# Kernel optimization log

Measured on AMD Instinct MI355X. Metric: run time of the kernel, lower is better.

## Reference

```python
import jax, jax.numpy as jnp
import numpy as np

EPS = 1e-5

def conv2d(x, w, stride=1, padding=0, bias=None):
    out = jax.lax.conv_general_dilated(
        x, w, (stride, stride), [(padding, padding), (padding, padding)],
        dimension_numbers=('NCHW', 'OIHW', 'NCHW'))
    if bias is not None:
        out = out + bias[None, :, None, None]
    return out

def bn_relu(x, gamma, beta, mean, var):
    scale = gamma / jnp.sqrt(var + EPS)
    return jax.nn.relu(x * scale[None, :, None, None]
                       + (beta - mean * scale)[None, :, None, None])

def deform_conv(x, wp, bp, wc, ks, pad, stride):
    # Canonical DeformConv2d (v1, modulation=False) from pytorch-deform-conv-v2.
    b, c, H, W = x.shape
    N = ks * ks
    offset = conv2d(x, wp, stride=stride, padding=1, bias=bp)        # (b,2N,h,w)
    h, w = offset.shape[2], offset.shape[3]
    xp = jnp.pad(x, ((0, 0), (0, 0), (pad, pad), (pad, pad)))        # zero_padding
    Hp, Wp = H + 2 * pad, W + 2 * pad
    off = offset.transpose(0, 2, 3, 1)                               # (b,h,w,2N)
    rng = jnp.arange(-(ks - 1) // 2, (ks - 1) // 2 + 1, dtype=x.dtype)
    pnx, pny = jnp.meshgrid(rng, rng, indexing='ij')
    pnx, pny = pnx.reshape(-1), pny.reshape(-1)                      # (N,)
    p0x = jnp.arange(1, h * stride + 1, stride, dtype=x.dtype)       # torch starts at 1
    p0y = jnp.arange(1, w * stride + 1, stride, dtype=x.dtype)
    px = p0x[None, :, None, None] + pnx[None, None, None, :] + off[..., :N]  # (b,h,w,N)
    py = p0y[None, None, :, None] + pny[None, None, None, :] + off[..., N:]
    qx0 = jnp.floor(jax.lax.stop_gradient(px))
    qy0 = jnp.floor(jax.lax.stop_gradient(py))
    qx0c = jnp.clip(qx0, 0, Hp - 1).astype(jnp.int32)
    qx1c = jnp.clip(qx0 + 1, 0, Hp - 1).astype(jnp.int32)
    qy0c = jnp.clip(qy0, 0, Wp - 1).astype(jnp.int32)
    qy1c = jnp.clip(qy0 + 1, 0, Wp - 1).astype(jnp.int32)
    pxc = jnp.clip(px, 0, Hp - 1)
    pyc = jnp.clip(py, 0, Wp - 1)
    fx0 = qx0c.astype(x.dtype); fx1 = qx1c.astype(x.dtype)
    fy0 = qy0c.astype(x.dtype); fy1 = qy1c.astype(x.dtype)
    g_lt = (1 + (fx0 - pxc)) * (1 + (fy0 - pyc))
    g_rb = (1 - (fx1 - pxc)) * (1 - (fy1 - pyc))
    g_lb = (1 + (fx0 - pxc)) * (1 - (fy1 - pyc))
    g_rt = (1 - (fx1 - pxc)) * (1 + (fy0 - pyc))
    xf = xp.reshape(b, c, Hp * Wp)
    def gather(qx, qy):
        idx = (qx * Wp + qy).reshape(b, 1, h * w * N)
        return jnp.take_along_axis(xf, idx, axis=2).reshape(b, c, h, w, N)
    x_off = (g_lt[:, None] * gather(qx0c, qy0c)
             + g_rb[:, None] * gather(qx1c, qy1c)
             + g_lb[:, None] * gather(qx0c, qy1c)
             + g_rt[:, None] * gather(qx1c, qy0c))                   # (b,c,h,w,N)
    # stride=ks conv over the reshaped (h*ks, w*ks) map == einsum over sample slot n
    return jnp.einsum('bchwn,ocn->bohw', x_off, wc.reshape(wc.shape[0], c, N))

def setup_inputs() -> dict:
    key = jax.random.key(0)
    ks = iter(jax.random.split(key, 40))
    def nrm(shape, scale):
        return jax.random.normal(next(ks), shape, dtype=jnp.float32) * scale
    def he(shape):  # fan_in = prod of all but first dim
        return nrm(shape, float(np.sqrt(2.0 / np.prod(shape[1:]))))
    def bn(c):
        return (jnp.ones((c,), jnp.float32) + nrm((c,), 0.05),  # gamma
                nrm((c,), 0.05),                                 # beta
                nrm((c,), 0.1),                                  # running mean
                jax.random.uniform(next(ks), (c,), jnp.float32, 0.5, 1.5))  # var
    inp = {'x': jax.random.normal(next(ks), (256, 3, 32, 32), dtype=jnp.float32)}
    inp['w1'] = he((32, 3, 3, 3)); inp['b1'] = nrm((32,), 0.01)
    inp['g1'], inp['be1'], inp['m1'], inp['v1'] = bn(32)
    inp['wp2'] = nrm((18, 32, 3, 3), 0.01); inp['bp2'] = nrm((18,), 0.001)
    inp['wc2'] = he((64, 32, 3, 3))
    inp['g2'], inp['be2'], inp['m2'], inp['v2'] = bn(64)
    inp['wp3'] = nrm((18, 64, 3, 3), 0.01); inp['bp3'] = nrm((18,), 0.001)
    inp['wc3'] = he((128, 64, 3, 3))
    inp['g3'], inp['be3'], inp['m3'], inp['v3'] = bn(128)
    inp['wp4'] = nrm((18, 128, 3, 3), 0.01); inp['bp4'] = nrm((18,), 0.001)
    inp['wc4'] = he((128, 128, 3, 3))
    inp['g4'], inp['be4'], inp['m4'], inp['v4'] = bn(128)
    inp['wcls'] = nrm((100, 128), float(1.0 / np.sqrt(128)))
    inp['bcls'] = nrm((100,), 0.01)
    return inp

def reference(x, w1, b1, g1, be1, m1, v1,
              wp2, bp2, wc2, g2, be2, m2, v2,
              wp3, bp3, wc3, g3, be3, m3, v3,
              wp4, bp4, wc4, g4, be4, m4, v4,
              wcls, bcls):
    h = bn_relu(conv2d(x, w1, stride=1, padding=1, bias=b1), g1, be1, m1, v1)   # (b,32,32,32)
    h = bn_relu(deform_conv(h, wp2, bp2, wc2, 3, 1, 2), g2, be2, m2, v2)        # (b,64,16,16)
    h = bn_relu(deform_conv(h, wp3, bp3, wc3, 3, 1, 1), g3, be3, m3, v3)        # (b,128,16,16)
    h = bn_relu(deform_conv(h, wp4, bp4, wc4, 3, 1, 2), g4, be4, m4, v4)        # (b,128,8,8)
    h = jnp.mean(h, axis=(2, 3))                                                # avg_pool2d(8) -> (b,128)
    return h @ wcls.T + bcls[None, :]
```

## Files before the change

### kernel.cpp

```cpp
#include <hip/hip_runtime.h>
#include <math.h>

#define BN_EPS 1e-5f

typedef __attribute__((ext_vector_type(4))) float f4;
typedef __attribute__((ext_vector_type(4))) int i4v;
typedef __attribute__((ext_vector_type(8))) short short8;
typedef __attribute__((ext_vector_type(4))) float f32x4;
typedef _Float16 half4v __attribute__((ext_vector_type(4)));

__device__ inline unsigned short f2bf(float f) {
    unsigned int u = __builtin_bit_cast(unsigned int, f);
    return (unsigned short)((u + 0x7FFFu + ((u >> 16) & 1u)) >> 16);
}
__device__ inline float blo(int u) { return __builtin_bit_cast(float, (int)(u << 16)); }
__device__ inline float bhi(int u) { return __builtin_bit_cast(float, (int)(u & 0xffff0000)); }
__device__ inline int pkbf_fast(float hi, float lo) {
    unsigned uh = __builtin_bit_cast(unsigned, hi) + 0x8000u;
    unsigned ul = __builtin_bit_cast(unsigned, lo) + 0x8000u;
    return (int)__builtin_amdgcn_perm(uh, ul, 0x07060302u);
}

struct CvtSeg { const float* src; unsigned short* dst; int oreal, c, kpad, end; };
struct CvtArgs { CvtSeg s[7]; };

__global__ __launch_bounds__(256)
void cvt_all(CvtArgs a)
{
    int idx = blockIdx.x * 256 + threadIdx.x;
    int base = 0;
    #pragma unroll
    for (int i = 0; i < 7; ++i) {
        if (idx < a.s[i].end) {
            int local = idx - base;
            int kpad = a.s[i].kpad, c = a.s[i].c;
            int o = local / kpad, k = local - o * kpad;
            unsigned short val = 0;
            if (o < a.s[i].oreal && k < 9 * c) {
                int n = k / c, cc = k - n * c;
                val = f2bf(a.s[i].src[(o * c + cc) * 9 + n]);
            }
            a.s[i].dst[local] = val;
            return;
        }
        base = a.s[i].end;
    }
}

__global__ __launch_bounds__(256)
void conv1_tile(const float* __restrict__ x, const unsigned short* __restrict__ wq,
                const float* __restrict__ bias, const float* __restrict__ g,
                const float* __restrict__ be, const float* __restrict__ m,
                const float* __restrict__ v, unsigned short* __restrict__ out)
{
    __shared__ __align__(16) float img[3072];
    __shared__ __align__(16) unsigned short wt[32 * 40];
    __shared__ float scb[32], shb[32];
    const int tid = threadIdx.x;
    const int b = blockIdx.x >> 2;
    const int qtr = blockIdx.x & 3;
    if (tid < 32) {
        float sc = g[tid] * rsqrtf(v[tid] + BN_EPS);
        scb[tid] = sc;
        shb[tid] = be[tid] - m[tid] * sc + bias[tid] * sc;
    }
    *(ushort4*)&wt[(tid >> 3) * 40 + (tid & 7) * 4] =
        *(const ushort4*)(wq + (tid >> 3) * 32 + (tid & 7) * 4);
    const float* xb = x + (size_t)b * 3072;
    #pragma unroll
    for (int r = 0; r < 3; ++r) {
        int idx = r * 256 + tid;
        *(f4*)&img[idx * 4] = *(const f4*)(xb + idx * 4);
    }
    __syncthreads();
    const int wid = tid >> 6, lane = tid & 63, quad = lane >> 4, m16 = lane & 15;
    short8 af0 = *(const short8*)&wt[m16 * 40 + quad * 8];
    short8 af1 = *(const short8*)&wt[(16 + m16) * 40 + quad * 8];
    #pragma unroll
    for (int it = 0; it < 4; ++it) {
        int pix = qtr * 256 + it * 64 + wid * 16 + m16;
        int i = pix >> 5, j = pix & 31;
        short8 bfrag;
        #pragma unroll
        for (int jj = 0; jj < 8; ++jj) {
            int k = quad * 8 + jj;
            float val = 0.f;
            if (k < 27) {
                int n = k / 3, c = k - n * 3;
                int u = i - 1 + n / 3, vv = j - 1 + n % 3;
                if (u >= 0 && u < 32 && vv >= 0 && vv < 32)
                    val = img[c * 1024 + u * 32 + vv];
            }
            bfrag[jj] = (short)f2bf(val);
        }
        f32x4 a0 = {0.f,0.f,0.f,0.f}, a1 = {0.f,0.f,0.f,0.f};
        a0 = __builtin_amdgcn_mfma_f32_16x16x32_bf16(af0, bfrag, a0, 0, 0, 0);
        a1 = __builtin_amdgcn_mfma_f32_16x16x32_bf16(af1, bfrag, a1, 0, 0, 0);
        unsigned short* op = out + ((size_t)b * 1024 + pix) * 32;
        ushort4 s0, s1;
        #pragma unroll
        for (int rr = 0; rr < 4; ++rr) {
            int o0 = quad * 4 + rr, o1 = 16 + quad * 4 + rr;
            ((unsigned short*)&s0)[rr] = f2bf(fmaxf(fmaf(a0[rr], scb[o0], shb[o0]), 0.f));
            ((unsigned short*)&s1)[rr] = f2bf(fmaxf(fmaf(a1[rr], scb[o1], shb[o1]), 0.f));
        }
        *(ushort4*)(op + quad * 4) = s0;
        *(ushort4*)(op + 16 + quad * 4) = s1;
    }
}

template<int C, int OREAL, int OPAD, int H, int W, int OH, int OW, int S, int MTILE>
__global__ __launch_bounds__(256, 4)
void dconv_slim(const unsigned short* __restrict__ xact,
                const unsigned short* __restrict__ wp, const float* __restrict__ bp,
                const unsigned short* __restrict__ wc,
                const float* __restrict__ g, const float* __restrict__ be,
                const float* __restrict__ m, const float* __restrict__ v,
                unsigned short* __restrict__ out)
{
    constexpr int K = C * 9;
    constexpr int KCH = C / 32;
    constexpr int OT = OPAD / 64;
    constexpr int ST = MTILE / 16;
    constexpr int PWP = MTILE / 2;
    constexpr int STP = PWP / 16;
    constexpr int CP = C + 8;
    constexpr int GL = C / 8;
    constexpr int NGRP = 256 / GL;
    constexpr int NT = MTILE / NGRP;
    constexpr int OHW = OH * OW;
    constexpr int HWC = H * W * C;
    constexpr int Hp = H + 2, Wpp = W + 2;
    static_assert(MTILE % NGRP == 0 && OPAD % 64 == 0 && STP >= 1, "tiling");

    __shared__ __align__(16) unsigned short xo[2][MTILE * CP];
    __shared__ __align__(8) ushort4   tab_p[MTILE][9];
    __shared__ __align__(8) _Float16  tab_h[MTILE][9][4];
    __shared__ _Float16 off_lds[MTILE][20];
    __shared__ int imgb[MTILE];
    __shared__ float scb[OPAD], shb[OPAD];

    const int tid = threadIdx.x;
    const int p0 = blockIdx.x * MTILE;

    if (tid < MTILE) imgb[tid] = ((p0 + tid) / OHW) * HWC;
    for (int o = tid; o < OREAL; o += 256) {
        float sc = g[o] * rsqrtf(v[o] + BN_EPS);
        scb[o] = sc;
        shb[o] = be[o] - m[o] * sc;
    }
    for (int e = tid; e < MTILE * 9; e += 256) {
        int lp = e / 9, n = e % 9;
        int p = p0 + lp;
        int rem = p % OHW;
        int i = rem / OW, j = rem % OW;
        int u = i * S - 1 + n / 3, vv = j * S - 1 + n % 3;
        bool ok = (u >= 0 && u < H && vv >= 0 && vv < W);
        ushort4 tp;
        tp.x = ok ? (unsigned short)((u * W + vv) * C) : (unsigned short)0;
        tp.y = ok ? (unsigned short)0xFFFF : (unsigned short)0;
        tp.z = 0; tp.w = 0;
        tab_p[lp][n] = tp;
    }
    __syncthreads();

    const int gl = tid % GL, grp = tid / GL;
    const int wid = tid >> 6, lane = tid & 63, quad = lane >> 4, m16 = lane & 15;

    {
        const int ogp = wid & 1;
        const int pgp = wid >> 1;
        const int obp = ogp * 16;
        const int pbp = pgp * PWP;
        i4v Tp[NT];
        auto issueA = [&](int n) {
            #pragma unroll
            for (int it = 0; it < NT; ++it) {
                const int pix = it * NGRP + grp;
                Tp[it] = *(const i4v*)(xact + imgb[pix] + gl * 8 + (int)tab_p[pix][n].x);
            }
        };
        auto commitA = [&](int n, int buf) {
            #pragma unroll
            for (int it = 0; it < NT; ++it) {
                const int pix = it * NGRP + grp;
                int mask = (int)(short)tab_p[pix][n].y;
                i4v R;
                #pragma unroll
                for (int e2 = 0; e2 < 4; ++e2) R[e2] = Tp[it][e2] & mask;
                *(i4v*)&xo[buf][pix * CP + gl * 8] = R;
            }
        };
        auto loadWp = [&](int n, short8* wf) {
            #pragma unroll
            for (int ch = 0; ch < KCH; ++ch)
                wf[ch] = *(const short8*)(wp + (size_t)(obp + m16) * K
                                          + n * C + ch * 32 + quad * 8);
        };
        f32x4 accp[STP];
        #pragma unroll
        for (int st = 0; st < STP; ++st) accp[st] = (f32x4){0.f, 0.f, 0.f, 0.f};
        short8 wfA[KCH], wfB[KCH];
        issueA(0);
        loadWp(0, wfA);
        commitA(0, 0);
        __syncthreads();
        for (int n = 0; n < 9; ++n) {
            const int cur = n & 1;
            if (n < 8) { issueA(n + 1); loadWp(n + 1, wfB); }
            #pragma unroll
            for (int ch = 0; ch < KCH; ++ch)
                #pragma unroll
                for (int st = 0; st < STP; ++st) {
                    short8 bf = *(const short8*)&xo[cur][(pbp + st * 16 + m16) * CP
                                                        + ch * 32 + quad * 8];
                    accp[st] = __builtin_amdgcn_mfma_f32_16x16x32_bf16(
                        wfA[ch], bf, accp[st], 0, 0, 0);
                }
            if (n < 8) {
                commitA(n + 1, cur ^ 1);
                #pragma unroll
                for (int ch = 0; ch < KCH; ++ch) wfA[ch] = wfB[ch];
            }
            __syncthreads();
        }
        #pragma unroll
        for (int st = 0; st < STP; ++st) {
            int pix = pbp + st * 16 + m16;
            #pragma unroll
            for (int rr = 0; rr < 4; ++rr) {
                int o = obp + quad * 4 + rr;
                if (o < 18) off_lds[pix][o] = (_Float16)(accp[st][rr] + bp[o]);
            }
        }
    }
    __syncthreads();

    for (int e = tid; e < MTILE * 9; e += 256) {
        int lp = e / 9, n = e % 9;
        int p = p0 + lp;
        int rem = p % OHW;
        int i = rem / OW, j = rem % OW;
        float ox = (float)off_lds[lp][n];
        float oy = (float)off_lds[lp][9 + n];
        float px = (float)(i * S + n / 3) + ox;
        float py = (float)(j * S + n % 3) + oy;
        int qx0 = (int)floorf(px), qy0 = (int)floorf(py);
        int x0 = min(max(qx0, 0), Hp - 1), x1 = min(max(qx0 + 1, 0), Hp - 1);
        int y0 = min(max(qy0, 0), Wpp - 1), y1 = min(max(qy0 + 1, 0), Wpp - 1);
        float pxc = fminf(fmaxf(px, 0.f), (float)(Hp - 1));
        float pyc = fminf(fmaxf(py, 0.f), (float)(Wpp - 1));
        float gx0 = 1.f + ((float)x0 - pxc), gx1 = 1.f - ((float)x1 - pxc);
        float gy0 = 1.f + ((float)y0 - pyc), gy1 = 1.f - ((float)y1 - pyc);
        int u0 = x0 - 1, u1 = x1 - 1, v0 = y0 - 1, v1 = y1 - 1;
        bool k0 = (u0 >= 0 && u0 < H && v0 >= 0 && v0 < W);
        bool k1 = (u1 >= 0 && u1 < H && v1 >= 0 && v1 < W);
        bool k2 = (u0 >= 0 && u0 < H && v1 >= 0 && v1 < W);
        bool k3 = (u1 >= 0 && u1 < H && v0 >= 0 && v0 < W);
        ushort4 tp;
        tp.x = k0 ? (unsigned short)((u0 * W + v0) * C) : (unsigned short)0;
        tp.y = k1 ? (unsigned short)((u1 * W + v1) * C) : (unsigned short)0;
        tp.z = k2 ? (unsigned short)((u0 * W + v1) * C) : (unsigned short)0;
        tp.w = k3 ? (unsigned short)((u1 * W + v0) * C) : (unsigned short)0;
        tab_p[lp][n] = tp;
        half4v hw;
        hw[0] = (_Float16)(k0 ? gx0 * gy0 : 0.f);
        hw[1] = (_Float16)(k1 ? gx1 * gy1 : 0.f);
        hw[2] = (_Float16)(k2 ? gx0 * gy1 : 0.f);
        hw[3] = (_Float16)(k3 ? gx1 * gy0 : 0.f);
        *(half4v*)&tab_h[lp][n][0] = hw;
    }
    __syncthreads();

    {
        const int obase = wid * OT * 16;
        i4v T[NT][4];
        auto issueC = [&](int n) {
            #pragma unroll
            for (int it = 0; it < NT; ++it) {
                const int pix = it * NGRP + grp;
                const unsigned short* xb = xact + imgb[pix] + gl * 8;
                ushort4 tp = tab_p[pix][n];
                T[it][0] = *(const i4v*)(xb + tp.x);
                T[it][1] = *(const i4v*)(xb + tp.y);
                T[it][2] = *(const i4v*)(xb + tp.z);
                T[it][3] = *(const i4v*)(xb + tp.w);
            }
        };
        auto commitC = [&](int n, int buf) {
            #pragma unroll
            for (int it = 0; it < NT; ++it) {
                const int pix = it * NGRP + grp;
                half4v hw = *(const half4v*)&tab_h[pix][n][0];
                float w0 = (float)hw[0], w1 = (float)hw[1];
                float w2 = (float)hw[2], w3 = (float)hw[3];
                i4v R;
                #pragma unroll
                for (int e2 = 0; e2 < 4; ++e2) {
                    float lo = w0 * blo(T[it][0][e2]);
                    lo = fmaf(w1, blo(T[it][1][e2]), lo);
                    lo = fmaf(w2, blo(T[it][2][e2]), lo);
                    lo = fmaf(w3, blo(T[it][3][e2]), lo);
                    float hi = w0 * bhi(T[it][0][e2]);
                    hi = fmaf(w1, bhi(T[it][1][e2]), hi);
                    hi = fmaf(w2, bhi(T[it][2][e2]), hi);
                    hi = fmaf(w3, bhi(T[it][3][e2]), hi);
                    R[e2] = pkbf_fast(hi, lo);
                }
                *(i4v*)&xo[buf][pix * CP + gl * 8] = R;
            }
        };
        auto loadWc = [&](int n, short8 (*wf)[OT]) {
            #pragma unroll
            for (int ch = 0; ch < KCH; ++ch)
                #pragma unroll
                for (int t = 0; t < OT; ++t)
                    wf[ch][t] = *(const short8*)(wc + (size_t)(obase + t * 16 + m16) * K
                                                 + n * C + ch * 32 + quad * 8);
        };

        f32x4 acc[ST][OT];
        #pragma unroll
        for (int st = 0; st < ST; ++st)
            #pragma unroll
            for (int t = 0; t < OT; ++t) acc[st][t] = (f32x4){0.f, 0.f, 0.f, 0.f};

        short8 wfA[KCH][OT], wfB[KCH][OT];
        issueC(0);
        loadWc(0, wfA);
        commitC(0, 0);
        __syncthreads();

        for (int n = 0; n < 9; ++n) {
            const int cur = n & 1;
            if (n < 8) {
                issueC(n + 1);
                loadWc(n + 1, wfB);
            }
            #pragma unroll
            for (int ch = 0; ch < KCH; ++ch)
                #pragma unroll
                for (int st = 0; st < ST; ++st) {
                    short8 bf = *(const short8*)&xo[cur][(st * 16 + m16) * CP
                                                        + ch * 32 + quad * 8];
                    #pragma unroll
                    for (int t = 0; t < OT; ++t)
                        acc[st][t] = __builtin_amdgcn_mfma_f32_16x16x32_bf16(
                            wfA[ch][t], bf, acc[st][t], 0, 0, 0);
                }
            if (n < 8) {
                commitC(n + 1, cur ^ 1);
                #pragma unroll
                for (int ch = 0; ch < KCH; ++ch)
                    #pragma unroll
                    for (int t = 0; t < OT; ++t) wfA[ch][t] = wfB[ch][t];
            }
            __syncthreads();
        }

        #pragma unroll
        for (int st = 0; st < ST; ++st) {
            const int p = p0 + st * 16 + m16;
            #pragma unroll
            for (int t = 0; t < OT; ++t) {
                int o = obase + t * 16 + quad * 4;
                ushort4 s;
                #pragma unroll
                for (int rr = 0; rr < 4; ++rr)
                    ((unsigned short*)&s)[rr] =
                        f2bf(fmaxf(fmaf(acc[st][t][rr], scb[o + rr], shb[o + rr]), 0.f));
                *(ushort4*)(out + (size_t)p * OPAD + o) = s;
            }
        }
    }
}

template<int C, int OREAL, int OPAD, int H, int W, int OH, int OW, int S, int MTILE>
__global__ __launch_bounds__(256, 3)
void dconv_fat(const unsigned short* __restrict__ xact,
               const unsigned short* __restrict__ wp, const float* __restrict__ bp,
               const unsigned short* __restrict__ wc,
               const float* __restrict__ g, const float* __restrict__ be,
               const float* __restrict__ m, const float* __restrict__ v,
               unsigned short* __restrict__ out)
{
    constexpr int K = C * 9;
    constexpr int KCH = C / 32;
    constexpr int OT = OPAD / 64;
    constexpr int ST = MTILE / 16;
    constexpr int PWP = MTILE / 2;
    constexpr int STP = PWP / 16;
    constexpr int CP = C + 8;
    constexpr int GL = C / 8;
    constexpr int NGRP = 256 / GL;
    constexpr int NT = MTILE / NGRP;
    constexpr int OHW = OH * OW;
    constexpr int HWC = H * W * C;
    constexpr int Hp = H + 2, Wpp = W + 2;
    static_assert(MTILE % NGRP == 0 && OPAD % 64 == 0, "tiling");

    __shared__ __align__(16) unsigned short xo[2][MTILE * CP];
    __shared__ __align__(16) i4v tab_i[MTILE][9];
    __shared__ __align__(16) f4  tab_w[MTILE][9];
    __shared__ int tab_o[MTILE][9];
    __shared__ int tab_m[MTILE][9];
    __shared__ float off_lds[MTILE][20];
    __shared__ int imgb[MTILE];
    __shared__ float scb[OPAD], shb[OPAD];

    const int tid = threadIdx.x;
    const int p0 = blockIdx.x * MTILE;

    if (tid < MTILE) imgb[tid] = ((p0 + tid) / OHW) * HWC;
    for (int o = tid; o < OREAL; o += 256) {
        float sc = g[o] * rsqrtf(v[o] + BN_EPS);
        scb[o] = sc;
        shb[o] = be[o] - m[o] * sc;
    }
    for (int e = tid; e < MTILE * 9; e += 256) {
        int lp = e / 9, n = e % 9;
        int p = p0 + lp;
        int rem = p % OHW;
        int i = rem / OW, j = rem % OW;
        int u = i * S - 1 + n / 3, vv = j * S - 1 + n % 3;
        bool ok = (u >= 0 && u < H && vv >= 0 && vv < W);
        tab_o[lp][n] = ok ? (u * W + vv) * C : 0;
        tab_m[lp][n] = ok ? -1 : 0;
    }
    __syncthreads();

    const int gl = tid % GL, grp = tid / GL;
    const int wid = tid >> 6, lane = tid & 63, quad = lane >> 4, m16 = lane & 15;

    {
        const int ogp = wid & 1, pgp = wid >> 1;
        const int obp = ogp * 16;
        const int pbp = pgp * PWP;
        i4v Tp[NT];
        auto issueA = [&](int n) {
            #pragma unroll
            for (int it = 0; it < NT; ++it) {
                const int pix = it * NGRP + grp;
                Tp[it] = *(const i4v*)(xact + imgb[pix] + gl * 8 + tab_o[pix][n]);
            }
        };
        auto commitA = [&](int n, int buf) {
            #pragma unroll
            for (int it = 0; it < NT; ++it) {
                const int pix = it * NGRP + grp;
                int mask = tab_m[pix][n];
                i4v R;
                #pragma unroll
                for (int e2 = 0; e2 < 4; ++e2) R[e2] = Tp[it][e2] & mask;
                *(i4v*)&xo[buf][pix * CP + gl * 8] = R;
            }
        };
        auto loadWp = [&](int n, short8* wf) {
            #pragma unroll
            for (int ch = 0; ch < KCH; ++ch)
                wf[ch] = *(const short8*)(wp + (size_t)(obp + m16) * K
                                          + n * C + ch * 32 + quad * 8);
        };
        f32x4 accp[STP];
        #pragma unroll
        for (int st = 0; st < STP; ++st) accp[st] = (f32x4){0.f, 0.f, 0.f, 0.f};
        short8 wfA[KCH], wfB[KCH];
        issueA(0);
        loadWp(0, wfA);
        commitA(0, 0);
        __syncthreads();
        for (int n = 0; n < 9; ++n) {
            const int cur = n & 1;
            if (n < 8) { issueA(n + 1); loadWp(n + 1, wfB); }
            #pragma unroll
            for (int ch = 0; ch < KCH; ++ch)
                #pragma unroll
                for (int st = 0; st < STP; ++st) {
                    short8 bf = *(const short8*)&xo[cur][(pbp + st * 16 + m16) * CP
                                                        + ch * 32 + quad * 8];
                    accp[st] = __builtin_amdgcn_mfma_f32_16x16x32_bf16(
                        wfA[ch], bf, accp[st], 0, 0, 0);
                }
            if (n < 8) {
                commitA(n + 1, cur ^ 1);
                #pragma unroll
                for (int ch = 0; ch < KCH; ++ch) wfA[ch] = wfB[ch];
            }
            __syncthreads();
        }
        #pragma unroll
        for (int st = 0; st < STP; ++st) {
            int pix = pbp + st * 16 + m16;
            #pragma unroll
            for (int rr = 0; rr < 4; ++rr) {
                int o = obp + quad * 4 + rr;
                if (o < 18) off_lds[pix][o] = accp[st][rr] + bp[o];
            }
        }
    }
    __syncthreads();

    for (int e = tid; e < MTILE * 9; e += 256) {
        int lp = e / 9, n = e % 9;
        int p = p0 + lp;
        int rem = p % OHW;
        int i = rem / OW, j = rem % OW;
        float ox = off_lds[lp][n];
        float oy = off_lds[lp][9 + n];
        float px = (float)(i * S + n / 3) + ox;
        float py = (float)(j * S + n % 3) + oy;
        int qx0 = (int)floorf(px), qy0 = (int)floorf(py);
        int x0 = min(max(qx0, 0), Hp - 1), x1 = min(max(qx0 + 1, 0), Hp - 1);
        int y0 = min(max(qy0, 0), Wpp - 1), y1 = min(max(qy0 + 1, 0), Wpp - 1);
        float pxc = fminf(fmaxf(px, 0.f), (float)(Hp - 1));
        float pyc = fminf(fmaxf(py, 0.f), (float)(Wpp - 1));
        float gx0 = 1.f + ((float)x0 - pxc), gx1 = 1.f - ((float)x1 - pxc);
        float gy0 = 1.f + ((float)y0 - pyc), gy1 = 1.f - ((float)y1 - pyc);
        int u0 = x0 - 1, u1 = x1 - 1, v0 = y0 - 1, v1 = y1 - 1;
        bool k0 = (u0 >= 0 && u0 < H && v0 >= 0 && v0 < W);
        bool k1 = (u1 >= 0 && u1 < H && v1 >= 0 && v1 < W);
        bool k2 = (u0 >= 0 && u0 < H && v1 >= 0 && v1 < W);
        bool k3 = (u1 >= 0 && u1 < H && v0 >= 0 && v0 < W);
        i4v ti; f4 tw;
        ti[0] = k0 ? (u0 * W + v0) * C : 0;  tw[0] = k0 ? gx0 * gy0 : 0.f;
        ti[1] = k1 ? (u1 * W + v1) * C : 0;  tw[1] = k1 ? gx1 * gy1 : 0.f;
        ti[2] = k2 ? (u0 * W + v1) * C : 0;  tw[2] = k2 ? gx0 * gy1 : 0.f;
        ti[3] = k3 ? (u1 * W + v0) * C : 0;  tw[3] = k3 ? gx1 * gy0 : 0.f;
        tab_i[lp][n] = ti;
        tab_w[lp][n] = tw;
    }
    __syncthreads();

    {
        const int obase = wid * OT * 16;
        i4v T[NT][4];
        auto issueC = [&](int n) {
            #pragma unroll
            for (int it = 0; it < NT; ++it) {
                const int pix = it * NGRP + grp;
                const unsigned short* xb = xact + imgb[pix] + gl * 8;
                i4v ti = tab_i[pix][n];
                T[it][0] = *(const i4v*)(xb + ti[0]);
                T[it][1] = *(const i4v*)(xb + ti[1]);
                T[it][2] = *(const i4v*)(xb + ti[2]);
                T[it][3] = *(const i4v*)(xb + ti[3]);
            }
        };
        auto commitC = [&](int n, int buf) {
            #pragma unroll
            for (int it = 0; it < NT; ++it) {
                const int pix = it * NGRP + grp;
                f4 tw = tab_w[pix][n];
                i4v R;
                #pragma unroll
                for (int e2 = 0; e2 < 4; ++e2) {
                    float lo = tw[0] * blo(T[it][0][e2]);
                    lo = fmaf(tw[1], blo(T[it][1][e2]), lo);
                    lo = fmaf(tw[2], blo(T[it][2][e2]), lo);
                    lo = fmaf(tw[3], blo(T[it][3][e2]), lo);
                    float hi = tw[0] * bhi(T[it][0][e2]);
                    hi = fmaf(tw[1], bhi(T[it][1][e2]), hi);
                    hi = fmaf(tw[2], bhi(T[it][2][e2]), hi);
                    hi = fmaf(tw[3], bhi(T[it][3][e2]), hi);
                    R[e2] = pkbf_fast(hi, lo);
                }
                *(i4v*)&xo[buf][pix * CP + gl * 8] = R;
            }
        };
        auto loadWc = [&](int n, short8 (*wf)[OT]) {
            #pragma unroll
            for (int ch = 0; ch < KCH; ++ch)
                #pragma unroll
                for (int t = 0; t < OT; ++t)
                    wf[ch][t] = *(const short8*)(wc + (size_t)(obase + t * 16 + m16) * K
                                                 + n * C + ch * 32 + quad * 8);
        };

        f32x4 acc[ST][OT];
        #pragma unroll
        for (int st = 0; st < ST; ++st)
            #pragma unroll
            for (int t = 0; t < OT; ++t) acc[st][t] = (f32x4){0.f, 0.f, 0.f, 0.f};

        short8 wfA[KCH][OT], wfB[KCH][OT];
        issueC(0);
        loadWc(0, wfA);
        commitC(0, 0);
        __syncthreads();

        for (int n = 0; n < 9; ++n) {
            const int cur = n & 1;
            if (n < 8) {
                issueC(n + 1);
                loadWc(n + 1, wfB);
            }
            #pragma unroll
            for (int ch = 0; ch < KCH; ++ch)
                #pragma unroll
                for (int st = 0; st < ST; ++st) {
                    short8 bf = *(const short8*)&xo[cur][(st * 16 + m16) * CP
                                                        + ch * 32 + quad * 8];
                    #pragma unroll
                    for (int t = 0; t < OT; ++t)
                        acc[st][t] = __builtin_amdgcn_mfma_f32_16x16x32_bf16(
                            wfA[ch][t], bf, acc[st][t], 0, 0, 0);
                }
            if (n < 8) {
                commitC(n + 1, cur ^ 1);
                #pragma unroll
                for (int ch = 0; ch < KCH; ++ch)
                    #pragma unroll
                    for (int t = 0; t < OT; ++t) wfA[ch][t] = wfB[ch][t];
            }
            __syncthreads();
        }

        #pragma unroll
        for (int st = 0; st < ST; ++st) {
            const int p = p0 + st * 16 + m16;
            #pragma unroll
            for (int t = 0; t < OT; ++t) {
                int o = obase + t * 16 + quad * 4;
                ushort4 s;
                #pragma unroll
                for (int rr = 0; rr < 4; ++rr)
                    ((unsigned short*)&s)[rr] =
                        f2bf(fmaxf(fmaf(acc[st][t][rr], scb[o + rr], shb[o + rr]), 0.f));
                *(ushort4*)(out + (size_t)p * OPAD + o) = s;
            }
        }
    }
}

__global__ __launch_bounds__(128)
void pool_fc(const unsigned short* __restrict__ h4, const float* __restrict__ wcls,
             const float* __restrict__ bcls, float* __restrict__ out)
{
    __shared__ float pool[128];
    int b = blockIdx.x;
    int tid = threadIdx.x;
    const unsigned short* src = h4 + (size_t)b * 8192;
    float s = 0.f;
    #pragma unroll
    for (int t = 0; t < 64; ++t)
        s += __builtin_bit_cast(float, (unsigned)src[t * 128 + tid] << 16);
    pool[tid] = s * (1.f / 64.f);
    __syncthreads();
    if (tid < 100) {
        float acc = bcls[tid];
        const float* wr = wcls + tid * 128;
        #pragma unroll
        for (int c = 0; c < 128; ++c) acc = fmaf(pool[c], wr[c], acc);
        out[(size_t)b * 100 + tid] = acc;
    }
}

extern "C" void kernel_launch(void* const* d_in, const int* in_sizes, int n_in,
                              void* d_out, int out_size, void* d_ws, size_t ws_size,
                              hipStream_t stream)
{
    const float* x    = (const float*)d_in[0];
    const float* w1   = (const float*)d_in[1];
    const float* b1   = (const float*)d_in[2];
    const float* g1   = (const float*)d_in[3];
    const float* be1  = (const float*)d_in[4];
    const float* m1   = (const float*)d_in[5];
    const float* v1   = (const float*)d_in[6];
    const float* wp2  = (const float*)d_in[7];
    const float* bp2  = (const float*)d_in[8];
    const float* wc2  = (const float*)d_in[9];
    const float* g2   = (const float*)d_in[10];
    const float* be2  = (const float*)d_in[11];
    const float* m2   = (const float*)d_in[12];
    const float* v2   = (const float*)d_in[13];
    const float* wp3  = (const float*)d_in[14];
    const float* bp3  = (const float*)d_in[15];
    const float* wc3  = (const float*)d_in[16];
    const float* g3   = (const float*)d_in[17];
    const float* be3  = (const float*)d_in[18];
    const float* m3   = (const float*)d_in[19];
    const float* v3   = (const float*)d_in[20];
    const float* wp4  = (const float*)d_in[21];
    const float* bp4  = (const float*)d_in[22];
    const float* wc4  = (const float*)d_in[23];
    const float* g4   = (const float*)d_in[24];
    const float* be4  = (const float*)d_in[25];
    const float* m4   = (const float*)d_in[26];
    const float* v4   = (const float*)d_in[27];
    const float* wcls = (const float*)d_in[28];
    const float* bcls = (const float*)d_in[29];
    float* out = (float*)d_out;

    unsigned short* h1 = (unsigned short*)d_ws;
    unsigned short* h2 = h1 + 8388608;
    unsigned short* h3 = h2 + 4194304;
    unsigned short* h4 = h3 + 8388608;
    unsigned short* wc2b = h4 + 2097152;
    unsigned short* wc3b = wc2b + 18432;
    unsigned short* wc4b = wc3b + 73728;
    unsigned short* wp2b = wc4b + 147456;
    unsigned short* wp3b = wp2b + 9216;
    unsigned short* wp4b = wp3b + 18432;
    unsigned short* wq1  = wp4b + 36864;
    (void)ws_size; (void)in_sizes; (void)n_in; (void)out_size;

    CvtArgs ca;
    ca.s[0] = { wc2, wc2b, 64, 32, 288, 18432 };
    ca.s[1] = { wc3, wc3b, 128, 64, 576, 92160 };
    ca.s[2] = { wc4, wc4b, 128, 128, 1152, 239616 };
    ca.s[3] = { wp2, wp2b, 18, 32, 288, 248832 };
    ca.s[4] = { wp3, wp3b, 18, 64, 576, 267264 };
    ca.s[5] = { wp4, wp4b, 18, 128, 1152, 304128 };
    ca.s[6] = { w1, wq1, 32, 3, 32, 305152 };
    cvt_all<<<1192, 256, 0, stream>>>(ca);

    conv1_tile<<<1024, 256, 0, stream>>>(x, wq1, b1, g1, be1, m1, v1, h1);

    dconv_slim<32, 64, 64, 32, 32, 16, 16, 2, 64><<<1024, 256, 0, stream>>>(
        h1, wp2b, bp2, wc2b, g2, be2, m2, v2, h2);

    dconv_slim<64, 128, 128, 16, 16, 16, 16, 1, 64><<<1024, 256, 0, stream>>>(
        h2, wp3b, bp3, wc3b, g3, be3, m3, v3, h3);

    dconv_fat<128, 128, 128, 16, 16, 8, 8, 2, 32><<<512, 256, 0, stream>>>(
        h3, wp4b, bp4, wc4b, g4, be4, m4, v4, h4);

    pool_fc<<<256, 128, 0, stream>>>(h4, wcls, bcls, out);
}
```

Before: 228.4 us.

## Split last deform conv over kernel taps across two blocks, fuse BN into pool

```diff
diff --git a/kernel.cpp b/kernel.cpp
--- a/kernel.cpp
+++ b/kernel.cpp
@@ -375,18 +375,16 @@
     }
 }
 
-template<int C, int OREAL, int OPAD, int H, int W, int OH, int OW, int S, int MTILE>
-__global__ __launch_bounds__(256, 3)
-void dconv_fat(const unsigned short* __restrict__ xact,
-               const unsigned short* __restrict__ wp, const float* __restrict__ bp,
-               const unsigned short* __restrict__ wc,
-               const float* __restrict__ g, const float* __restrict__ be,
-               const float* __restrict__ m, const float* __restrict__ v,
-               unsigned short* __restrict__ out)
+template<int C, int O, int H, int W, int OH, int OW, int S, int MTILE>
+__global__ __launch_bounds__(256, 4)
+void dconv_ks(const unsigned short* __restrict__ xact,
+              const unsigned short* __restrict__ wp, const float* __restrict__ bp,
+              const unsigned short* __restrict__ wc,
+              float* __restrict__ out0, float* __restrict__ out1)
 {
     constexpr int K = C * 9;
     constexpr int KCH = C / 32;
-    constexpr int OT = OPAD / 64;
+    constexpr int OT = O / 64;
     constexpr int ST = MTILE / 16;
     constexpr int PWP = MTILE / 2;
     constexpr int STP = PWP / 16;
@@ -397,26 +395,21 @@
     constexpr int OHW = OH * OW;
     constexpr int HWC = H * W * C;
     constexpr int Hp = H + 2, Wpp = W + 2;
-    static_assert(MTILE % NGRP == 0 && OPAD % 64 == 0, "tiling");
 
     __shared__ __align__(16) unsigned short xo[2][MTILE * CP];
-    __shared__ __align__(16) i4v tab_i[MTILE][9];
-    __shared__ __align__(16) f4  tab_w[MTILE][9];
-    __shared__ int tab_o[MTILE][9];
-    __shared__ int tab_m[MTILE][9];
-    __shared__ float off_lds[MTILE][20];
+    __shared__ __align__(8) ushort4   tab_p[MTILE][9];
+    __shared__ __align__(8) _Float16  tab_h[MTILE][9][4];
+    __shared__ _Float16 off_lds[MTILE][20];
     __shared__ int imgb[MTILE];
-    __shared__ float scb[OPAD], shb[OPAD];
 
     const int tid = threadIdx.x;
-    const int p0 = blockIdx.x * MTILE;
+    const int ob = blockIdx.x & 1;
+    const int p0 = (blockIdx.x >> 1) * MTILE;
+    const int nlo = ob ? 5 : 0;
+    const int nhi = ob ? 9 : 5;
+    float* outp = ob ? out1 : out0;
 
     if (tid < MTILE) imgb[tid] = ((p0 + tid) / OHW) * HWC;
-    for (int o = tid; o < OREAL; o += 256) {
-        float sc = g[o] * rsqrtf(v[o] + BN_EPS);
-        scb[o] = sc;
-        shb[o] = be[o] - m[o] * sc;
-    }
     for (int e = tid; e < MTILE * 9; e += 256) {
         int lp = e / 9, n = e % 9;
         int p = p0 + lp;
@@ -424,8 +417,11 @@
         int i = rem / OW, j = rem % OW;
         int u = i * S - 1 + n / 3, vv = j * S - 1 + n % 3;
         bool ok = (u >= 0 && u < H && vv >= 0 && vv < W);
-        tab_o[lp][n] = ok ? (u * W + vv) * C : 0;
-        tab_m[lp][n] = ok ? -1 : 0;
+        ushort4 tp;
+        tp.x = ok ? (unsigned short)((u * W + vv) * C) : (unsigned short)0;
+        tp.y = ok ? (unsigned short)0xFFFF : (unsigned short)0;
+        tp.z = 0; tp.w = 0;
+        tab_p[lp][n] = tp;
     }
     __syncthreads();
 
@@ -433,7 +429,8 @@
     const int wid = tid >> 6, lane = tid & 63, quad = lane >> 4, m16 = lane & 15;
 
     {
-        const int ogp = wid & 1, pgp = wid >> 1;
+        const int ogp = wid & 1;
+        const int pgp = wid >> 1;
         const int obp = ogp * 16;
         const int pbp = pgp * PWP;
         i4v Tp[NT];
@@ -441,14 +438,14 @@
             #pragma unroll
             for (int it = 0; it < NT; ++it) {
                 const int pix = it * NGRP + grp;
-                Tp[it] = *(const i4v*)(xact + imgb[pix] + gl * 8 + tab_o[pix][n]);
+                Tp[it] = *(const i4v*)(xact + imgb[pix] + gl * 8 + (int)tab_p[pix][n].x);
             }
         };
         auto commitA = [&](int n, int buf) {
             #pragma unroll
             for (int it = 0; it < NT; ++it) {
                 const int pix = it * NGRP + grp;
-                int mask = tab_m[pix][n];
+                int mask = (int)(short)tab_p[pix][n].y;
                 i4v R;
                 #pragma unroll
                 for (int e2 = 0; e2 < 4; ++e2) R[e2] = Tp[it][e2] & mask;
@@ -494,7 +491,7 @@
             #pragma unroll
             for (int rr = 0; rr < 4; ++rr) {
                 int o = obp + quad * 4 + rr;
-                if (o < 18) off_lds[pix][o] = accp[st][rr] + bp[o];
+                if (o < 18) off_lds[pix][o] = (_Float16)(accp[st][rr] + bp[o]);
             }
         }
     }
@@ -502,11 +499,12 @@
 
     for (int e = tid; e < MTILE * 9; e += 256) {
         int lp = e / 9, n = e % 9;
+        if (n < nlo || n >= nhi) continue;
         int p = p0 + lp;
         int rem = p % OHW;
         int i = rem / OW, j = rem % OW;
-        float ox = off_lds[lp][n];
-        float oy = off_lds[lp][9 + n];
+        float ox = (float)off_lds[lp][n];
+        float oy = (float)off_lds[lp][9 + n];
         float px = (float)(i * S + n / 3) + ox;
         float py = (float)(j * S + n % 3) + oy;
         int qx0 = (int)floorf(px), qy0 = (int)floorf(py);
@@ -521,13 +519,18 @@
         bool k1 = (u1 >= 0 && u1 < H && v1 >= 0 && v1 < W);
         bool k2 = (u0 >= 0 && u0 < H && v1 >= 0 && v1 < W);
         bool k3 = (u1 >= 0 && u1 < H && v0 >= 0 && v0 < W);
-        i4v ti; f4 tw;
-        ti[0] = k0 ? (u0 * W + v0) * C : 0;  tw[0] = k0 ? gx0 * gy0 : 0.f;
-        ti[1] = k1 ? (u1 * W + v1) * C : 0;  tw[1] = k1 ? gx1 * gy1 : 0.f;
-        ti[2] = k2 ? (u0 * W + v1) * C : 0;  tw[2] = k2 ? gx0 * gy1 : 0.f;
-        ti[3] = k3 ? (u1 * W + v0) * C : 0;  tw[3] = k3 ? gx1 * gy0 : 0.f;
-        tab_i[lp][n] = ti;
-        tab_w[lp][n] = tw;
+        ushort4 tp;
+        tp.x = k0 ? (unsigned short)((u0 * W + v0) * C) : (unsigned short)0;
+        tp.y = k1 ? (unsigned short)((u1 * W + v1) * C) : (unsigned short)0;
+        tp.z = k2 ? (unsigned short)((u0 * W + v1) * C) : (unsigned short)0;
+        tp.w = k3 ? (unsigned short)((u1 * W + v0) * C) : (unsigned short)0;
+        tab_p[lp][n] = tp;
+        half4v hw;
+        hw[0] = (_Float16)(k0 ? gx0 * gy0 : 0.f);
+        hw[1] = (_Float16)(k1 ? gx1 * gy1 : 0.f);
+        hw[2] = (_Float16)(k2 ? gx0 * gy1 : 0.f);
+        hw[3] = (_Float16)(k3 ? gx1 * gy0 : 0.f);
+        *(half4v*)&tab_h[lp][n][0] = hw;
     }
     __syncthreads();
 
@@ -539,29 +542,31 @@
             for (int it = 0; it < NT; ++it) {
                 const int pix = it * NGRP + grp;
                 const unsigned short* xb = xact + imgb[pix] + gl * 8;
-                i4v ti = tab_i[pix][n];
-                T[it][0] = *(const i4v*)(xb + ti[0]);
-                T[it][1] = *(const i4v*)(xb + ti[1]);
-                T[it][2] = *(const i4v*)(xb + ti[2]);
-                T[it][3] = *(const i4v*)(xb + ti[3]);
+                ushort4 tp = tab_p[pix][n];
+                T[it][0] = *(const i4v*)(xb + tp.x);
+                T[it][1] = *(const i4v*)(xb + tp.y);
+                T[it][2] = *(const i4v*)(xb + tp.z);
+                T[it][3] = *(const i4v*)(xb + tp.w);
             }
         };
         auto commitC = [&](int n, int buf) {
             #pragma unroll
             for (int it = 0; it < NT; ++it) {
                 const int pix = it * NGRP + grp;
-                f4 tw = tab_w[pix][n];
+                half4v hw = *(const half4v*)&tab_h[pix][n][0];
+                float w0 = (float)hw[0], w1 = (float)hw[1];
+                float w2 = (float)hw[2], w3 = (float)hw[3];
                 i4v R;
                 #pragma unroll
                 for (int e2 = 0; e2 < 4; ++e2) {
-                    float lo = tw[0] * blo(T[it][0][e2]);
-                    lo = fmaf(tw[1], blo(T[it][1][e2]), lo);
-                    lo = fmaf(tw[2], blo(T[it][2][e2]), lo);
-                    lo = fmaf(tw[3], blo(T[it][3][e2]), lo);
-                    float hi = tw[0] * bhi(T[it][0][e2]);
-                    hi = fmaf(tw[1], bhi(T[it][1][e2]), hi);
-                    hi = fmaf(tw[2], bhi(T[it][2][e2]), hi);
-                    hi = fmaf(tw[3], bhi(T[it][3][e2]), hi);
+                    float lo = w0 * blo(T[it][0][e2]);
+                    lo = fmaf(w1, blo(T[it][1][e2]), lo);
+                    lo = fmaf(w2, blo(T[it][2][e2]), lo);
+                    lo = fmaf(w3, blo(T[it][3][e2]), lo);
+                    float hi = w0 * bhi(T[it][0][e2]);
+                    hi = fmaf(w1, bhi(T[it][1][e2]), hi);
+                    hi = fmaf(w2, bhi(T[it][2][e2]), hi);
+                    hi = fmaf(w3, bhi(T[it][3][e2]), hi);
                     R[e2] = pkbf_fast(hi, lo);
                 }
                 *(i4v*)&xo[buf][pix * CP + gl * 8] = R;
@@ -583,14 +588,14 @@
             for (int t = 0; t < OT; ++t) acc[st][t] = (f32x4){0.f, 0.f, 0.f, 0.f};
 
         short8 wfA[KCH][OT], wfB[KCH][OT];
-        issueC(0);
-        loadWc(0, wfA);
-        commitC(0, 0);
+        issueC(nlo);
+        loadWc(nlo, wfA);
+        commitC(nlo, 0);
         __syncthreads();
 
-        for (int n = 0; n < 9; ++n) {
-            const int cur = n & 1;
-            if (n < 8) {
+        for (int n = nlo; n < nhi; ++n) {
+            const int cur = (n - nlo) & 1;
+            if (n + 1 < nhi) {
                 issueC(n + 1);
                 loadWc(n + 1, wfB);
             }
@@ -605,7 +610,7 @@
                         acc[st][t] = __builtin_amdgcn_mfma_f32_16x16x32_bf16(
                             wfA[ch][t], bf, acc[st][t], 0, 0, 0);
                 }
-            if (n < 8) {
+            if (n + 1 < nhi) {
                 commitC(n + 1, cur ^ 1);
                 #pragma unroll
                 for (int ch = 0; ch < KCH; ++ch)
@@ -621,29 +626,35 @@
             #pragma unroll
             for (int t = 0; t < OT; ++t) {
                 int o = obase + t * 16 + quad * 4;
-                ushort4 s;
-                #pragma unroll
-                for (int rr = 0; rr < 4; ++rr)
-                    ((unsigned short*)&s)[rr] =
-                        f2bf(fmaxf(fmaf(acc[st][t][rr], scb[o + rr], shb[o + rr]), 0.f));
-                *(ushort4*)(out + (size_t)p * OPAD + o) = s;
+                f4 r;
+                #pragma unroll
+                for (int rr = 0; rr < 4; ++rr) r[rr] = acc[st][t][rr];
+                *(f4*)(outp + (size_t)p * O + o) = r;
             }
         }
     }
 }
 
 __global__ __launch_bounds__(128)
-void pool_fc(const unsigned short* __restrict__ h4, const float* __restrict__ wcls,
-             const float* __restrict__ bcls, float* __restrict__ out)
+void pool_fc_ks(const float* __restrict__ h4a, const float* __restrict__ h4b,
+                const float* __restrict__ g, const float* __restrict__ be,
+                const float* __restrict__ m, const float* __restrict__ v,
+                const float* __restrict__ wcls, const float* __restrict__ bcls,
+                float* __restrict__ out)
 {
     __shared__ float pool[128];
     int b = blockIdx.x;
     int tid = threadIdx.x;
-    const unsigned short* src = h4 + (size_t)b * 8192;
+    float sc = g[tid] * rsqrtf(v[tid] + BN_EPS);
+    float sh = be[tid] - m[tid] * sc;
+    const float* pa = h4a + (size_t)b * 8192 + tid;
+    const float* pb = h4b + (size_t)b * 8192 + tid;
     float s = 0.f;
     #pragma unroll
-    for (int t = 0; t < 64; ++t)
-        s += __builtin_bit_cast(float, (unsigned)src[t * 128 + tid] << 16);
+    for (int t = 0; t < 64; ++t) {
+        float val = pa[t * 128] + pb[t * 128];
+        s += fmaxf(fmaf(val, sc, sh), 0.f);
+    }
     pool[tid] = s * (1.f / 64.f);
     __syncthreads();
     if (tid < 100) {
@@ -694,8 +705,9 @@
     unsigned short* h1 = (unsigned short*)d_ws;
     unsigned short* h2 = h1 + 8388608;
     unsigned short* h3 = h2 + 4194304;
-    unsigned short* h4 = h3 + 8388608;
-    unsigned short* wc2b = h4 + 2097152;
+    float* h4a = (float*)(h3 + 8388608);
+    float* h4b = h4a + 2097152;
+    unsigned short* wc2b = (unsigned short*)(h4b + 2097152);
     unsigned short* wc3b = wc2b + 18432;
     unsigned short* wc4b = wc3b + 73728;
     unsigned short* wp2b = wc4b + 147456;
@@ -722,8 +734,8 @@
     dconv_slim<64, 128, 128, 16, 16, 16, 16, 1, 64><<<1024, 256, 0, stream>>>(
         h2, wp3b, bp3, wc3b, g3, be3, m3, v3, h3);
 
-    dconv_fat<128, 128, 128, 16, 16, 8, 8, 2, 32><<<512, 256, 0, stream>>>(
-        h3, wp4b, bp4, wc4b, g4, be4, m4, v4, h4);
-
-    pool_fc<<<256, 128, 0, stream>>>(h4, wcls, bcls, out);
+    dconv_ks<128, 128, 16, 16, 8, 8, 2, 32><<<1024, 256, 0, stream>>>(
+        h3, wp4b, bp4, wc4b, h4a, h4b);
+
+    pool_fc_ks<<<256, 128, 0, stream>>>(h4a, h4b, g4, be4, m4, v4, wcls, bcls, out);
 }
```

After: 246.6 us. 1.08x slower.
